# Kernel tuning notes

Measured on AMD Instinct MI355X. Metric: run time of the kernel, lower is better.

Reference implementation:

```python
import jax, jax.numpy as jnp
import numpy as np

CONF_THRESH = 0.25


def setup_inputs() -> dict:
    key = jax.random.key(0)
    # Raw YOLO head output: [batch, n_anchors, 4 box + 1 objectness + 80 classes]
    output = jax.random.uniform(key, (16, 25200, 85), dtype=jnp.float32)
    return {"output": output}


def reference(output):
    # Faithful JAX version of ModelWrapper._process_raw_output fallback path.
    # Torch emits a variable-length [M, 6] tensor; with static shapes we emit
    # the dense [B, N, 6] decoded boxes with below-threshold rows zeroed
    # (equivalent information: masked rows are exactly the dropped ones).
    box_xy = output[..., 0:2]            # [B, N, 2]
    box_wh = output[..., 2:4]            # [B, N, 2]
    box_conf = output[..., 4]            # [B, N]
    box_cls = output[..., 5:]            # [B, N, C]

    half_wh = box_wh * 0.5
    xy_min = box_xy - half_wh            # xmin, ymin
    xy_max = box_xy + half_wh            # xmax, ymax

    max_scores = jnp.max(box_cls, axis=-1)                    # [B, N]
    max_cls_idx = jnp.argmax(box_cls, axis=-1)                # [B, N]
    scores = box_conf * max_scores                            # [B, N]
    mask = scores > CONF_THRESH                               # [B, N]

    boxes = jnp.concatenate(
        [xy_min, xy_max, scores[..., None],
         max_cls_idx.astype(output.dtype)[..., None]], axis=-1)  # [B, N, 6]
    return jnp.where(mask[..., None], boxes, jnp.zeros((), dtype=output.dtype))
```

## Files before the change

kernel.cpp:

```cpp
#include <hip/hip_runtime.h>

#define ROWS_PER_BLOCK 128
#define THREADS 128
#define ROW_F 85
#define NCLS 80
#define CONF_THRESH 0.25f

__global__ __launch_bounds__(THREADS) void yolo_post_kernel(
    const float* __restrict__ in, float* __restrict__ out, int nrows) {
  __shared__ float tile[ROWS_PER_BLOCK * ROW_F];

  const long long row0 = (long long)blockIdx.x * ROWS_PER_BLOCK;
  const long long base_f = row0 * ROW_F;
  const long long total_f = (long long)nrows * ROW_F;

  const int tile_v = (ROWS_PER_BLOCK * ROW_F) / 4;
  const float4* __restrict__ src = (const float4*)(in + base_f);
  float4* dstv = (float4*)tile;
  for (int i = threadIdx.x; i < tile_v; i += THREADS) {
    if (base_f + (long long)i * 4 + 3 < total_f) {
      dstv[i] = src[i];
    }
  }
  __syncthreads();

  const long long r = row0 + threadIdx.x;
  if (r >= nrows) return;
  const float* row = tile + threadIdx.x * ROW_F;

  float cx = row[0];
  float cy = row[1];
  float hw = row[2] * 0.5f;
  float hh = row[3] * 0.5f;
  float conf = row[4];

  float best = row[5];
  int bidx = 0;
#pragma unroll
  for (int c = 1; c < NCLS; ++c) {
    float v = row[5 + c];
    bool gt = v > best;
    best = gt ? v : best;
    bidx = gt ? c : bidx;
  }

  float score = conf * best;
  bool keep = score > CONF_THRESH;

  float o0 = keep ? cx - hw : 0.0f;
  float o1 = keep ? cy - hh : 0.0f;
  float o2 = keep ? cx + hw : 0.0f;
  float o3 = keep ? cy + hh : 0.0f;
  float o4 = keep ? score : 0.0f;
  float o5 = keep ? (float)bidx : 0.0f;

  float* op = out + r * 6;
  op[0] = o0;
  op[1] = o1;
  op[2] = o2;
  op[3] = o3;
  op[4] = o4;
  op[5] = o5;
}

extern "C" void kernel_launch(void* const* d_in, const int* in_sizes, int n_in,
                              void* d_out, int out_size, void* d_ws, size_t ws_size,
                              hipStream_t stream) {
  const float* in = (const float*)d_in[0];
  float* out = (float*)d_out;
  const int nrows = in_sizes[0] / ROW_F;
  const int grid = (nrows + ROWS_PER_BLOCK - 1) / ROWS_PER_BLOCK;
  yolo_post_kernel<<<grid, THREADS, 0, stream>>>(in, out, nrows);
}
```

Measured before the change: 225.3 us.

## Drop LDS staging and read rows directly from global memory

Removes the shared-memory tile and barrier so each thread loads its 85-float row straight from global memory, and raises the block size to 256. It also writes outputs as three float2 stores instead of six scalars. The goal is to avoid LDS capacity limits on occupancy, LDS bank conflicts and the sync. The cost is strided, uncoalesced global loads across lanes, which rely on the cache to recover reuse.

```diff
diff --git a/kernel.cpp b/kernel.cpp
--- a/kernel.cpp
+++ b/kernel.cpp
@@ -1,32 +1,16 @@
 #include <hip/hip_runtime.h>
 
-#define ROWS_PER_BLOCK 128
-#define THREADS 128
 #define ROW_F 85
 #define NCLS 80
 #define CONF_THRESH 0.25f
+#define THREADS 256
 
 __global__ __launch_bounds__(THREADS) void yolo_post_kernel(
     const float* __restrict__ in, float* __restrict__ out, int nrows) {
-  __shared__ float tile[ROWS_PER_BLOCK * ROW_F];
+  const int r = blockIdx.x * THREADS + threadIdx.x;
+  if (r >= nrows) return;
 
-  const long long row0 = (long long)blockIdx.x * ROWS_PER_BLOCK;
-  const long long base_f = row0 * ROW_F;
-  const long long total_f = (long long)nrows * ROW_F;
-
-  const int tile_v = (ROWS_PER_BLOCK * ROW_F) / 4;
-  const float4* __restrict__ src = (const float4*)(in + base_f);
-  float4* dstv = (float4*)tile;
-  for (int i = threadIdx.x; i < tile_v; i += THREADS) {
-    if (base_f + (long long)i * 4 + 3 < total_f) {
-      dstv[i] = src[i];
-    }
-  }
-  __syncthreads();
-
-  const long long r = row0 + threadIdx.x;
-  if (r >= nrows) return;
-  const float* row = tile + threadIdx.x * ROW_F;
+  const float* __restrict__ row = in + (long long)r * ROW_F;
 
   float cx = row[0];
   float cy = row[1];
@@ -38,29 +22,23 @@
   int bidx = 0;
 #pragma unroll
   for (int c = 1; c < NCLS; ++c) {
-    float v = row[5 + c];
-    bool gt = v > best;
-    best = gt ? v : best;
-    bidx = gt ? c : bidx;
+    float x = row[5 + c];
+    bool g = x > best;
+    best = g ? x : best;
+    bidx = g ? c : bidx;
   }
 
   float score = conf * best;
   bool keep = score > CONF_THRESH;
 
-  float o0 = keep ? cx - hw : 0.0f;
-  float o1 = keep ? cy - hh : 0.0f;
-  float o2 = keep ? cx + hw : 0.0f;
-  float o3 = keep ? cy + hh : 0.0f;
-  float o4 = keep ? score : 0.0f;
-  float o5 = keep ? (float)bidx : 0.0f;
+  float2 o01 = keep ? make_float2(cx - hw, cy - hh) : make_float2(0.f, 0.f);
+  float2 o23 = keep ? make_float2(cx + hw, cy + hh) : make_float2(0.f, 0.f);
+  float2 o45 = keep ? make_float2(score, (float)bidx) : make_float2(0.f, 0.f);
 
-  float* op = out + r * 6;
-  op[0] = o0;
-  op[1] = o1;
-  op[2] = o2;
-  op[3] = o3;
-  op[4] = o4;
-  op[5] = o5;
+  float2* op = (float2*)(out + (long long)r * 6);
+  op[0] = o01;
+  op[1] = o23;
+  op[2] = o45;
 }
 
 extern "C" void kernel_launch(void* const* d_in, const int* in_sizes, int n_in,
@@ -69,6 +47,6 @@
   const float* in = (const float*)d_in[0];
   float* out = (float*)d_out;
   const int nrows = in_sizes[0] / ROW_F;
-  const int grid = (nrows + ROWS_PER_BLOCK - 1) / ROWS_PER_BLOCK;
+  const int grid = (nrows + THREADS - 1) / THREADS;
   yolo_post_kernel<<<grid, THREADS, 0, stream>>>(in, out, nrows);
 }
```

New measurement: 203.6 us. 1.11x faster.
